# Kernel optimization log

Measured on AMD Instinct MI355X. Metric: run time of the kernel, lower is better.

The kernel has to match this reference:

```python
import jax, jax.numpy as jnp
import numpy as np
from jax import lax

EPS = 1e-5

def conv3x3(x, w):
    # x: [B,C,H,W], w: [O,C,3,3]
    return lax.conv_general_dilated(x, w, (1, 1), ((1, 1), (1, 1)),
                                    dimension_numbers=("NCHW", "OIHW", "NCHW"))

def convbnrelu(x, w, bn):
    gamma, beta, mean, var = bn  # each [C]
    y = conv3x3(x, w)
    scale = (gamma / jnp.sqrt(var + EPS))[:, None, None]
    shift = (beta - mean * gamma / jnp.sqrt(var + EPS))[:, None, None]
    return jax.nn.relu(y * scale + shift)

def conv1x1(x, w, b):
    # w: [O,C,1,1], b: [O]
    return jnp.einsum("bchw,oc->bohw", x, w[:, :, 0, 0]) + b[:, None, None]

def pam(x, wb, bb, wc, bc, wd, bd, alpha, lfm=None):
    B, C, H, W = x.shape
    N = H * W
    q = conv1x1(x, wb, bb)
    k = conv1x1(x, wc, bc)
    v = conv1x1(x, wd, bd)
    if lfm is not None:  # VFAM: qkv flags all 1 -> multiply q, k, v
        q = q * lfm
        k = k * lfm
        v = v * lfm
    fb = q.reshape(B, -1, N).transpose(0, 2, 1)           # [B,N,Cq]
    fc = k.reshape(B, -1, N)                              # [B,Cq,N]
    attn = jax.nn.softmax(jnp.matmul(fb, fc), axis=-1)    # [B,N,N]
    fd = v.reshape(B, C, N)                               # [B,C,N]
    fe = jnp.matmul(fd, attn.transpose(0, 2, 1)).reshape(B, C, H, W)
    return alpha * fe + x

def cam(x, beta):
    B, C, H, W = x.shape
    N = H * W
    fa = x.reshape(B, C, N)
    attn = jnp.matmul(fa, fa.transpose(0, 2, 1))          # [B,C,C]
    attn = jnp.max(attn, axis=-1, keepdims=True) - attn
    attn = jax.nn.softmax(attn, axis=-1)
    fe = jnp.matmul(attn, fa).reshape(B, C, H, W)
    return beta * fe + x

def setup_inputs() -> dict:
    key = jax.random.key(0)
    ks = iter(jax.random.split(key, 64))
    B, Cin, H, W = 2, 2048, 64, 64
    Cmid = Cin // 4         # 512
    Cq = Cmid // 8          # 64
    nclass = 19

    def bn_pack(C):
        g = jnp.ones((C,)) + 0.1 * jax.random.normal(next(ks), (C,))
        b = 0.1 * jax.random.normal(next(ks), (C,))
        m = 0.1 * jax.random.normal(next(ks), (C,))
        v = jax.random.uniform(next(ks), (C,), minval=0.5, maxval=1.5)
        return jnp.stack([g, b, m, v])  # [4,C]

    def conv_w(O, I, kk):
        return jax.random.normal(next(ks), (O, I, kk, kk)) * (1.0 / np.sqrt(I * kk * kk))

    inp = {
        "x": jax.random.normal(next(ks), (B, Cin, H, W)),
        "loss_factor_map": jax.random.uniform(next(ks), (H, W)),
        "wp1": conv_w(Cmid, Cin, 3), "bnp1": bn_pack(Cmid),
        "wp2": conv_w(Cmid, Cmid, 3), "bnp2": bn_pack(Cmid),
        "wc1": conv_w(Cmid, Cin, 3), "bnc1": bn_pack(Cmid),
        "wc2": conv_w(Cmid, Cmid, 3), "bnc2": bn_pack(Cmid),
        "wv1": conv_w(Cmid, Cin, 3), "bnv1": bn_pack(Cmid),
        "wv2": conv_w(Cmid, Cmid, 3), "bnv2": bn_pack(Cmid),
        "pam_wb": conv_w(Cq, Cmid, 1), "pam_bb": jnp.zeros((Cq,)),
        "pam_wc": conv_w(Cq, Cmid, 1), "pam_bc": jnp.zeros((Cq,)),
        "pam_wd": conv_w(Cmid, Cmid, 1), "pam_bd": jnp.zeros((Cmid,)),
        "pam_alpha": 0.3 * jnp.ones((1,)),
        "cam_beta": 0.3 * jnp.ones((1,)),
        "vfam_wb": conv_w(Cq, Cmid, 1), "vfam_bb": jnp.zeros((Cq,)),
        "vfam_wc": conv_w(Cq, Cmid, 1), "vfam_bc": jnp.zeros((Cq,)),
        "vfam_wd": conv_w(Cmid, Cmid, 1), "vfam_bd": jnp.zeros((Cmid,)),
        "vfam_alpha": 0.3 * jnp.ones((1,)),
        "out_w": conv_w(nclass, Cmid, 1), "out_b": jnp.zeros((nclass,)),
        "p3_w": conv_w(nclass, Cmid, 1), "p3_b": jnp.zeros((nclass,)),
        "c3_w": conv_w(nclass, Cmid, 1), "c3_b": jnp.zeros((nclass,)),
    }
    return inp

def reference(x, loss_factor_map,
              wp1, bnp1, wp2, bnp2, wc1, bnc1, wc2, bnc2, wv1, bnv1, wv2, bnv2,
              pam_wb, pam_bb, pam_wc, pam_bc, pam_wd, pam_bd, pam_alpha,
              cam_beta,
              vfam_wb, vfam_bb, vfam_wc, vfam_bc, vfam_wd, vfam_bd, vfam_alpha,
              out_w, out_b, p3_w, p3_b, c3_w, c3_b):
    lfm = loss_factor_map[None, None, :, :]  # (1,1,H,W)
    # Position branch
    fp = convbnrelu(x, wp1, bnp1)
    fp = pam(fp, pam_wb, pam_bb, pam_wc, pam_bc, pam_wd, pam_bd, pam_alpha)
    fp = convbnrelu(fp, wp2, bnp2)
    # Channel branch
    fc = convbnrelu(x, wc1, bnc1)
    fc = cam(fc, cam_beta)
    fc = convbnrelu(fc, wc2, bnc2)
    # Visual-field branch (qkv_vfa_flag = [1,1,1])
    fv = convbnrelu(x, wv1, bnv1)
    fv = pam(fv, vfam_wb, vfam_bb, vfam_wc, vfam_bc, vfam_wd, vfam_bd, vfam_alpha, lfm=lfm)
    fv = convbnrelu(fv, wv2, bnv2)
    # Fusion + heads (Dropout in eval mode = identity)
    fusion = fp + fc + fv
    fusion_out = conv1x1(fusion, out_w, out_b)
    p_out = conv1x1(fp, p3_w, p3_b)
    c_out = conv1x1(fc, c3_w, c3_b)
    return (fusion_out, p_out, c_out)
```

## Files before the change

### kernel.cpp

```cpp
#include <hip/hip_runtime.h>

typedef unsigned short u16;
typedef short s16x8 __attribute__((ext_vector_type(8)));
typedef u16 u16x8 __attribute__((ext_vector_type(8)));
typedef u16 u16x4 __attribute__((ext_vector_type(4)));
typedef float f32x4 __attribute__((ext_vector_type(4)));

#define DEV __device__ __forceinline__

DEV float bf2f(u16 x) { unsigned v = ((unsigned)x) << 16; float f; __builtin_memcpy(&f, &v, 4); return f; }
DEV u16 f2bf(float f) { unsigned u; __builtin_memcpy(&u, &f, 4); u += 0x7FFFu + ((u >> 16) & 1u); return (u16)(u >> 16); }

DEV void gload16(const u16* g, u16* l) {
  __builtin_amdgcn_global_load_lds((const __attribute__((address_space(1))) void*)g,
                                   (__attribute__((address_space(3))) void*)l, 16, 0, 0);
}

__global__ void detect_dtype(const u16* __restrict__ x, int* __restrict__ flag) {
  int tid = threadIdx.x;
  float mx = 0.f;
  for (int i = tid; i < 4096; i += 256) mx = fmaxf(mx, fabsf(bf2f(x[i])));
  __shared__ float red[4];
  int wave = tid >> 6, lane = tid & 63;
  for (int off = 32; off; off >>= 1) mx = fmaxf(mx, __shfl_xor(mx, off));
  if (lane == 0) red[wave] = mx;
  __syncthreads();
  if (tid == 0) {
    mx = fmaxf(fmaxf(red[0], red[1]), fmaxf(red[2], red[3]));
    *flag = (mx > 1e4f) ? 1 : 0;
  }
}

struct CvBatch {
  const void* src[28];
  unsigned dstOff[28];
  unsigned n[28];
  unsigned chunkStart[29];
  int cnt;
};

__global__ __launch_bounds__(256) void convert_batch(CvBatch cb, u16* __restrict__ dstBase,
                                                     const int* __restrict__ flag) {
  const int isF = *flag;
  const unsigned bid = blockIdx.x;
  int j = 0;
  while (bid >= cb.chunkStart[j + 1]) ++j;
  const unsigned base = (bid - cb.chunkStart[j]) * 2048 + threadIdx.x * 8;
  const unsigned n = cb.n[j];
  if (base >= n) return;
  u16* dst = dstBase + cb.dstOff[j];
  const void* src = cb.src[j];
  if (base + 8 <= n) {
    u16x8 v;
    if (isF) {
      const float* f = (const float*)src;
#pragma unroll
      for (int k = 0; k < 8; ++k) v[k] = f2bf(f[base + k]);
    } else {
      v = *(const u16x8*)&((const u16*)src)[base];
    }
    *(u16x8*)&dst[base] = v;
  } else {
    for (unsigned i = base; i < n; ++i)
      dst[i] = isF ? f2bf(((const float*)src)[i]) : ((const u16*)src)[i];
  }
}

__global__ void bn_prep(const u16* __restrict__ cbn, float* __restrict__ out) {
  int w = blockIdx.x;
  const u16* bn = cbn + w * 2048;
  int c = threadIdx.x;
  float g = bf2f(bn[c]), be = bf2f(bn[512 + c]), m = bf2f(bn[1024 + c]), v = bf2f(bn[1536 + c]);
  float sc = g * rsqrtf(v + 1e-5f);
  out[w * 1024 + c] = sc;
  out[w * 1024 + 512 + c] = be - m * sc;
}

struct Repack3P { const void* src[3]; u16* dst[3]; };

__global__ __launch_bounds__(256) void repack_w3(Repack3P rp, int I, int Ishift,
                                                 const int* __restrict__ flag) {
  const int isF = *flag;
  const void* w = rp.src[blockIdx.z];
  u16* wr = rp.dst[blockIdx.z];
  size_t idx = ((size_t)blockIdx.x * 256 + threadIdx.x) * 8;
  int i0 = (int)(idx & (size_t)(I - 1));
  int t = (int)(idx >> Ishift);
  int o = t / 9, kk = t - o * 9;
  u16x8 v;
  if (isF) {
    const float* f = (const float*)w;
#pragma unroll
    for (int j = 0; j < 8; ++j) v[j] = f2bf(f[((size_t)o * I + i0 + j) * 9 + kk]);
  } else {
    const u16* bsrc = (const u16*)w;
#pragma unroll
    for (int j = 0; j < 8; ++j) v[j] = bsrc[((size_t)o * I + i0 + j) * 9 + kk];
  }
  *(u16x8*)&wr[idx] = v;
}

__global__ __launch_bounds__(256) void zero_border(u16* __restrict__ base, int CIN) {
  int p = blockIdx.x, b = blockIdx.y;
  int py, px;
  if (p < 66)       { py = 0;        px = p; }
  else if (p < 132) { py = 65;       px = p - 66; }
  else if (p < 196) { py = p - 131;  px = 0; }
  else              { py = p - 195;  px = 65; }
  u16* d = base + (((size_t)b * 66 + py) * 66 + px) * (size_t)CIN;
  for (int i = threadIdx.x * 8; i < CIN; i += 2048) {
    u16x8 z;
#pragma unroll
    for (int k = 0; k < 8; ++k) z[k] = 0;
    *(u16x8*)&d[i] = z;
  }
}

__global__ __launch_bounds__(256) void pad_nchw(const void* __restrict__ x, u16* __restrict__ xpad,
                                                const int* __restrict__ flag) {
  __shared__ u16 t[64][72];
  const int isF = *flag;
  int c0 = blockIdx.x * 64, h = blockIdx.y, b = blockIdx.z;
  int tid = threadIdx.x;
#pragma unroll
  for (int i = 0; i < 2; ++i) {
    int idx = i * 256 + tid;
    int cc = idx >> 3, ww = (idx & 7) * 8;
    size_t base = (((size_t)(b * 2048 + c0 + cc) * 64) + h) * 64 + ww;
    u16x8 v;
    if (isF) {
      const float* fx = (const float*)x;
#pragma unroll
      for (int j = 0; j < 8; ++j) v[j] = f2bf(fx[base + j]);
    } else {
      v = *(const u16x8*)&((const u16*)x)[base];
    }
    *(u16x8*)&t[cc][ww] = v;
  }
  __syncthreads();
#pragma unroll
  for (int i = 0; i < 2; ++i) {
    int idx = i * 256 + tid;
    int ww = idx >> 3, cc = (idx & 7) * 8;
    u16x8 v;
#pragma unroll
    for (int j = 0; j < 8; ++j) v[j] = t[cc + j][ww];
    *(u16x8*)&xpad[(((size_t)b * 66 + h + 1) * 66 + ww + 1) * 2048 + c0 + cc] = v;
  }
}

__global__ __launch_bounds__(256) void transpose64(const u16* __restrict__ src, u16* __restrict__ dst,
                                                   int R, int C) {
  __shared__ u16 t[64][72];
  int r0 = blockIdx.x * 64, c0 = blockIdx.y * 64;
  const u16* s = src + (size_t)blockIdx.z * R * C;
  u16* d = dst + (size_t)blockIdx.z * R * C;
  int tid = threadIdx.x;
#pragma unroll
  for (int i = 0; i < 2; ++i) {
    int idx = i * 256 + tid;
    int rr = idx >> 3, cc = (idx & 7) * 8;
    u16x8 v = *(const u16x8*)&s[(size_t)(r0 + rr) * C + c0 + cc];
    *(u16x8*)&t[rr][cc] = v;
  }
  __syncthreads();
#pragma unroll
  for (int i = 0; i < 2; ++i) {
    int idx = i * 256 + tid;
    int cc = idx >> 3, rr = (idx & 7) * 8;
    u16x8 v;
#pragma unroll
    for (int j = 0; j < 8; ++j) v[j] = t[rr + j][cc];
    *(u16x8*)&d[(size_t)(c0 + cc) * R + r0 + rr] = v;
  }
}

struct GemmP {
  const u16* A; const u16* B;
  long aBatch, bBatch;
  int M, N, K;
  u16* out; long outBatch; int ldOut;
  const u16* bias;
  const u16* rowscale;
  const u16* residual; long resBatch; int ldRes;
  const u16* alphaPtr;
  float* outF; long outFBatch;
  const u16* B2; const u16* bias2; u16* out2;
};

template <int BM, int BN, int EPI>
__global__ __launch_bounds__(256) void gemm_nt(GemmP p) {
  static_assert(EPI != 2 || BM >= BN, "EPI2 LDS bounce needs BM>=BN");
  __shared__ __align__(16) u16 lsBuf[(BM + BN) * 32];
  u16* lA = lsBuf;
  u16* lB = lsBuf + BM * 32;
  const int tid = threadIdx.x;
  int bz = blockIdx.z;
  const u16* Bsel = p.B;
  const u16* biasSel = p.bias;
  u16* outSel = p.out;
  if (EPI == 0 && p.out2) {
    const int h = gridDim.z >> 1;
    if (bz >= h) { bz -= h; Bsel = p.B2; biasSel = p.bias2; outSel = p.out2; }
  }
  const int m0 = blockIdx.x * BM, n0 = blockIdx.y * BN;
  const u16* A = p.A + (size_t)bz * p.aBatch;
  const u16* Bp = Bsel + (size_t)bz * p.bBatch;
  const int wave = tid >> 6, lane = tid & 63;
  const int quad = lane >> 4, r16 = lane & 15;
  const int wm = (wave >> 1) * (BM / 2), wn = (wave & 1) * (BN / 2);
  constexpr int TM = BM / 32, TN = BN / 32;
  f32x4 acc[TM][TN] = {};
  const int srow = tid >> 2, sch = (tid & 3) * 8;
  const int K = p.K;
  for (int k0 = 0; k0 < K; k0 += 32) {
    __syncthreads();
#pragma unroll
    for (int i = 0; i < BM / 64; ++i)
      gload16(&A[(size_t)(m0 + i * 64 + srow) * K + k0 + sch], lA + i * 2048 + wave * 512);
#pragma unroll
    for (int i = 0; i < BN / 64; ++i)
      gload16(&Bp[(size_t)(n0 + i * 64 + srow) * K + k0 + sch], lB + i * 2048 + wave * 512);
    __syncthreads();
    s16x8 av[TM], bv[TN];
#pragma unroll
    for (int t = 0; t < TM; ++t) av[t] = *(const s16x8*)&lA[(wm + t * 16 + r16) * 32 + quad * 8];
#pragma unroll
    for (int t = 0; t < TN; ++t) bv[t] = *(const s16x8*)&lB[(wn + t * 16 + r16) * 32 + quad * 8];
#pragma unroll
    for (int i = 0; i < TM; ++i)
#pragma unroll
      for (int j = 0; j < TN; ++j)
        acc[i][j] = __builtin_amdgcn_mfma_f32_16x16x32_bf16(av[i], bv[j], acc[i][j], 0, 0, 0);
  }
  if constexpr (EPI == 2) {
    float* lsF = (float*)lsBuf;
#pragma unroll
    for (int i = 0; i < TM; ++i) {
      __syncthreads();
#pragma unroll
      for (int j = 0; j < TN; ++j) {
        const int col = wn + j * 16 + r16;
#pragma unroll
        for (int r = 0; r < 4; ++r) {
          const int rowL = (wave >> 1) * 16 + quad * 4 + r;
          lsF[rowL * BN + col] = acc[i][j][r];
        }
      }
      __syncthreads();
      constexpr int PASSES = (32 * BN) / 1024;
#pragma unroll
      for (int pp = 0; pp < PASSES; ++pp) {
        const int lin = (pp * 256 + tid) * 4;
        const int rowL = lin / BN, col = lin & (BN - 1);
        const int gm = m0 + (rowL >> 4) * (BM / 2) + i * 16 + (rowL & 15);
        *(f32x4*)&p.outF[(size_t)bz * p.outFBatch + (size_t)gm * p.ldOut + (n0 + col)] =
            *(const f32x4*)&lsF[lin];
      }
    }
    return;
  }
  float alpha = 0.f;
  if (EPI == 3) alpha = bf2f(p.alphaPtr[0]);
#pragma unroll
  for (int i = 0; i < TM; ++i) {
#pragma unroll
    for (int j = 0; j < TN; ++j) {
      const int nn = n0 + wn + j * 16 + r16;
      float bia = 0.f;
      if ((EPI == 0 || EPI == 1) && biasSel) bia = bf2f(biasSel[nn]);
#pragma unroll
      for (int r = 0; r < 4; ++r) {
        const int mm = m0 + wm + i * 16 + quad * 4 + r;
        float v = acc[i][j][r];
        if (EPI == 0) {
          v += bia;
          if (p.rowscale) v *= bf2f(p.rowscale[mm]);
          outSel[(size_t)bz * p.outBatch + (size_t)mm * p.ldOut + nn] = f2bf(v);
        } else if (EPI == 1) {
          v += bia;
          if (p.rowscale) v *= bf2f(p.rowscale[mm]);
          p.out[(size_t)bz * p.outBatch + (size_t)nn * p.ldOut + mm] = f2bf(v);
        } else {
          float res = bf2f(p.residual[(size_t)bz * p.resBatch + (size_t)mm * p.ldRes + nn]);
          v = alpha * v + res;
          const int py = mm >> 6, px = mm & 63;
          p.out[(size_t)bz * p.outBatch + ((size_t)(py + 1) * 66 + (px + 1)) * p.ldOut + nn] = f2bf(v);
        }
      }
    }
  }
}

struct Conv3P {
  const u16* in[3];
  const u16* wr[3];
  u16* out[3];
  const float* bn;
};

template <int CIN>
__global__ __launch_bounds__(256) void conv3x3_k(Conv3P p) {
  __shared__ u16 lA[4096], lB[4096];
  const int tid = threadIdx.x;
  const int z = blockIdx.z, ci = z >> 1, b = z & 1;
  const int m0 = blockIdx.x * 128, n0 = blockIdx.y * 128;
  const u16* __restrict__ xin = p.in[ci];
  const u16* __restrict__ wr = p.wr[ci];
  const int wave = tid >> 6, lane = tid & 63;
  const int quad = lane >> 4, r16 = lane & 15;
  const int wm = (wave >> 1) * 64, wn = (wave & 1) * 64;
  f32x4 acc[4][4] = {};
  const int srow = tid >> 2, sch = (tid & 3) * 8;
  const int p0 = m0 + srow, p1 = p0 + 64;
  const size_t a0 = (((size_t)b * 66 + (p0 >> 6)) * 66 + (p0 & 63)) * CIN + sch;
  const size_t a1 = (((size_t)b * 66 + (p1 >> 6)) * 66 + (p1 & 63)) * CIN + sch;
  const size_t b0 = ((size_t)(n0 + srow) * 9) * CIN + sch;
  const size_t b1 = ((size_t)(n0 + 64 + srow) * 9) * CIN + sch;
  u16* la0 = &lA[wave * 512];
  u16* la1 = &lA[2048 + wave * 512];
  u16* lb0 = &lB[wave * 512];
  u16* lb1 = &lB[2048 + wave * 512];
  for (int kh = 0; kh < 3; ++kh) {
    for (int kw = 0; kw < 3; ++kw) {
      const size_t soff = ((size_t)kh * 66 + kw) * CIN;
      const size_t woff = (size_t)(kh * 3 + kw) * CIN;
      for (int c = 0; c < CIN; c += 32) {
        __syncthreads();
        gload16(&xin[a0 + soff + c], la0);
        gload16(&xin[a1 + soff + c], la1);
        gload16(&wr[b0 + woff + c], lb0);
        gload16(&wr[b1 + woff + c], lb1);
        __syncthreads();
        s16x8 av[4], bv[4];
#pragma unroll
        for (int t = 0; t < 4; ++t) av[t] = *(const s16x8*)&lA[(wm + t * 16 + r16) * 32 + quad * 8];
#pragma unroll
        for (int t = 0; t < 4; ++t) bv[t] = *(const s16x8*)&lB[(wn + t * 16 + r16) * 32 + quad * 8];
#pragma unroll
        for (int i = 0; i < 4; ++i)
#pragma unroll
          for (int j = 0; j < 4; ++j)
            acc[i][j] = __builtin_amdgcn_mfma_f32_16x16x32_bf16(av[i], bv[j], acc[i][j], 0, 0, 0);
      }
    }
  }
  u16* __restrict__ out = p.out[ci];
  const float* bnS = p.bn + ci * 1024;
#pragma unroll
  for (int i = 0; i < 4; ++i) {
#pragma unroll
    for (int j = 0; j < 4; ++j) {
      const int nn = n0 + wn + j * 16 + r16;
      const float s = bnS[nn], sh = bnS[512 + nn];
#pragma unroll
      for (int r = 0; r < 4; ++r) {
        const int mm = m0 + wm + i * 16 + quad * 4 + r;
        float v = fmaxf(acc[i][j][r] * s + sh, 0.f);
        out[((size_t)b * 4096 + mm) * 512 + nn] = f2bf(v);
      }
    }
  }
}

__global__ __launch_bounds__(256) void softmax4096(const float* __restrict__ S, u16* __restrict__ P) {
  int row = blockIdx.x, tid = threadIdx.x;
  const float* sr = S + (size_t)row * 4096;
  f32x4 v[4];
  float mx = -3.4e38f;
#pragma unroll
  for (int i = 0; i < 4; ++i) {
    v[i] = *(const f32x4*)&sr[(i * 256 + tid) * 4];
    mx = fmaxf(mx, fmaxf(fmaxf(v[i][0], v[i][1]), fmaxf(v[i][2], v[i][3])));
  }
  __shared__ float red[8];
  int wave = tid >> 6, lane = tid & 63;
  for (int off = 32; off; off >>= 1) mx = fmaxf(mx, __shfl_xor(mx, off));
  if (lane == 0) red[wave] = mx;
  __syncthreads();
  mx = fmaxf(fmaxf(red[0], red[1]), fmaxf(red[2], red[3]));
  float sum = 0.f;
#pragma unroll
  for (int i = 0; i < 4; ++i)
#pragma unroll
    for (int j = 0; j < 4; ++j) { float e = __expf(v[i][j] - mx); v[i][j] = e; sum += e; }
  for (int off = 32; off; off >>= 1) sum += __shfl_xor(sum, off);
  if (lane == 0) red[4 + wave] = sum;
  __syncthreads();
  sum = red[4] + red[5] + red[6] + red[7];
  float inv = 1.f / sum;
  u16* pr = P + (size_t)row * 4096;
#pragma unroll
  for (int i = 0; i < 4; ++i) {
    u16x4 ov;
#pragma unroll
    for (int j = 0; j < 4; ++j) ov[j] = f2bf(v[i][j] * inv);
    *(u16x4*)&pr[(i * 256 + tid) * 4] = ov;
  }
}

__global__ __launch_bounds__(256) void softmax_cam(const float* __restrict__ S, u16* __restrict__ P) {
  int row = blockIdx.x, tid = threadIdx.x;
  const float* sr = S + (size_t)row * 512;
  float a = sr[tid], b = sr[tid + 256];
  __shared__ float red[12];
  int wave = tid >> 6, lane = tid & 63;
  float mx = fmaxf(a, b);
  for (int off = 32; off; off >>= 1) mx = fmaxf(mx, __shfl_xor(mx, off));
  if (lane == 0) red[wave] = mx;
  __syncthreads();
  float M1 = fmaxf(fmaxf(red[0], red[1]), fmaxf(red[2], red[3]));
  float mn = fminf(a, b);
  for (int off = 32; off; off >>= 1) mn = fminf(mn, __shfl_xor(mn, off));
  if (lane == 0) red[4 + wave] = mn;
  __syncthreads();
  float m2 = M1 - fminf(fminf(red[4], red[5]), fminf(red[6], red[7]));
  float e0 = __expf((M1 - a) - m2), e1 = __expf((M1 - b) - m2);
  float sum = e0 + e1;
  for (int off = 32; off; off >>= 1) sum += __shfl_xor(sum, off);
  if (lane == 0) red[8 + wave] = sum;
  __syncthreads();
  sum = red[8] + red[9] + red[10] + red[11];
  float inv = 1.f / sum;
  P[(size_t)row * 512 + tid] = f2bf(e0 * inv);
  P[(size_t)row * 512 + tid + 256] = f2bf(e1 * inv);
}

__global__ __launch_bounds__(256) void final_out_k(const u16* __restrict__ fp2, const u16* __restrict__ fc2,
                                                   const u16* __restrict__ fv2,
                                                   const u16* ow, const u16* ob, const u16* pw,
                                                   const u16* pb, const u16* cw, const u16* cb,
                                                   void* __restrict__ out, const int* __restrict__ flag) {
  __shared__ float wl[19 * 512];
  int tid = threadIdx.x, which = blockIdx.y;
  const u16* W = which == 0 ? ow : which == 1 ? pw : cw;
  const u16* Bb = which == 0 ? ob : which == 1 ? pb : cb;
  for (int i = tid; i < 19 * 512; i += 256) wl[i] = bf2f(W[i]);
  __syncthreads();
  int pix = blockIdx.x * 256 + threadIdx.x;
  size_t rb = (size_t)pix * 512;
  float acc[19];
#pragma unroll
  for (int o = 0; o < 19; ++o) acc[o] = 0.f;
  for (int c = 0; c < 512; c += 8) {
    float xs[8];
    if (which == 0) {
      u16x8 a = *(const u16x8*)&fp2[rb + c];
      u16x8 d = *(const u16x8*)&fc2[rb + c];
      u16x8 e = *(const u16x8*)&fv2[rb + c];
#pragma unroll
      for (int j = 0; j < 8; ++j) xs[j] = bf2f(a[j]) + bf2f(d[j]) + bf2f(e[j]);
    } else {
      const u16* src = which == 1 ? fp2 : fc2;
      u16x8 a = *(const u16x8*)&src[rb + c];
#pragma unroll
      for (int j = 0; j < 8; ++j) xs[j] = bf2f(a[j]);
    }
#pragma unroll
    for (int o = 0; o < 19; ++o) {
      const float* wv = &wl[o * 512 + c];
#pragma unroll
      for (int j = 0; j < 8; ++j) acc[o] += xs[j] * wv[j];
    }
  }
  int b = pix >> 12, n = pix & 4095;
  const int isF32 = *flag;
#pragma unroll
  for (int o = 0; o < 19; ++o) {
    size_t idx = (size_t)which * 155648 + ((size_t)(b * 19 + o)) * 4096 + n;
    float v = acc[o] + bf2f(Bb[o]);
    if (isF32) ((float*)out)[idx] = v;
    else ((u16*)out)[idx] = f2bf(v);
  }
}

static const size_t OFF_XPAD  = 0;
static const size_t OFF_WR1A  = 35684352;
static const size_t OFF_WR1B  = 54558720;
static const size_t OFF_WR1C  = 73433088;
static const size_t OFF_ARENA = 92307456;
static const size_t OFF_S     = 0;
static const size_t OFF_P     = 67108864;
static const size_t OFF_FP1   = 125861888;
static const size_t OFF_FC1   = 134250496;
static const size_t OFF_FV1   = 142639104;
static const size_t OFF_FC1T  = 151027712;
static const size_t OFF_QT    = 159416320;
static const size_t OFF_KT    = 160464896;
static const size_t OFF_VT    = 161513472;
static const size_t OFF_WRSA  = 151027712;
static const size_t OFF_WRSB  = 155746304;
static const size_t OFF_WRSC  = 161513472;
static const size_t OFF_PADP  = 169902080;
static const size_t OFF_PADC  = 178823168;
static const size_t OFF_PADV  = 187744256;
static const size_t OFF_FP2   = 125861888;
static const size_t OFF_FC2   = 134250496;
static const size_t OFF_FV2   = 142639104;
static const size_t OFF_SC    = 196665344;
static const size_t OFF_PC    = 198762496;
static const size_t OFF_BN    = 199811072;
static const size_t OFF_FLAG  = 199835648;
static const size_t OFF_SMALL = 199835904;
static const size_t SO_CBN    = 0;
static const size_t SO_PWB    = 12288;
static const size_t SO_PBB    = 45056;
static const size_t SO_PWC    = 45120;
static const size_t SO_PBC    = 77888;
static const size_t SO_PWD    = 77952;
static const size_t SO_PBD    = 340096;
static const size_t SO_PAL    = 340608;
static const size_t SO_CBETA  = 340624;
static const size_t SO_VWB    = 340640;
static const size_t SO_VBB    = 373408;
static const size_t SO_VWC    = 373472;
static const size_t SO_VBC    = 406240;
static const size_t SO_VWD    = 406304;
static const size_t SO_VBD    = 668448;
static const size_t SO_VAL    = 668960;
static const size_t SO_OW     = 668976;
static const size_t SO_OB     = 678704;
static const size_t SO_PW3    = 678736;
static const size_t SO_PB3    = 688464;
static const size_t SO_CW3    = 688496;
static const size_t SO_CB3    = 698224;
static const size_t SO_LFM    = 698256;
static const size_t SO_END    = 702352;
static const size_t WS_NEEDED = OFF_SMALL + SO_END * 2;

extern "C" void kernel_launch(void* const* d_in, const int* in_sizes, int n_in,
                              void* d_out, int out_size, void* d_ws, size_t ws_size,
                              hipStream_t stream) {
  if (ws_size < WS_NEEDED) return;
  (void)in_sizes; (void)n_in; (void)out_size;

  char* ws = (char*)d_ws;
  u16* xpad   = (u16*)(ws + OFF_XPAD);
  u16* wr1a   = (u16*)(ws + OFF_WR1A);
  u16* wr1b   = (u16*)(ws + OFF_WR1B);
  u16* wr1c   = (u16*)(ws + OFF_WR1C);
  float* S    = (float*)(ws + OFF_S);
  u16* P      = (u16*)(ws + OFF_P);
  u16* fp1    = (u16*)(ws + OFF_FP1);
  u16* fc1    = (u16*)(ws + OFF_FC1);
  u16* fv1    = (u16*)(ws + OFF_FV1);
  u16* fc1T   = (u16*)(ws + OFF_FC1T);
  u16* qt     = (u16*)(ws + OFF_QT);
  u16* kt     = (u16*)(ws + OFF_KT);
  u16* vT     = (u16*)(ws + OFF_VT);
  u16* wrsa   = (u16*)(ws + OFF_WRSA);
  u16* wrsb   = (u16*)(ws + OFF_WRSB);
  u16* wrsc   = (u16*)(ws + OFF_WRSC);
  u16* padP   = (u16*)(ws + OFF_PADP);
  u16* padC   = (u16*)(ws + OFF_PADC);
  u16* padV   = (u16*)(ws + OFF_PADV);
  u16* fp2    = (u16*)(ws + OFF_FP2);
  u16* fc2    = (u16*)(ws + OFF_FC2);
  u16* fv2    = (u16*)(ws + OFF_FV2);
  float* Sc   = (float*)(ws + OFF_SC);
  u16* Pc     = (u16*)(ws + OFF_PC);
  float* bnb  = (float*)(ws + OFF_BN);
  int* flag   = (int*)(ws + OFF_FLAG);
  u16* sm     = (u16*)(ws + OFF_SMALL);

  detect_dtype<<<1, 256, 0, stream>>>((const u16*)d_in[0], flag);
  {
    CvBatch cb{};
    int jn = 0; unsigned chunks = 0;
    auto addJob = [&](int i, size_t dstOff, unsigned n) {
      cb.src[jn] = d_in[i]; cb.dstOff[jn] = (unsigned)dstOff; cb.n[jn] = n;
      cb.chunkStart[jn] = chunks; chunks += (n + 2047) / 2048; ++jn;
    };
    addJob(3,  SO_CBN + 0 * 2048, 2048);
    addJob(7,  SO_CBN + 1 * 2048, 2048);
    addJob(11, SO_CBN + 2 * 2048, 2048);
    addJob(5,  SO_CBN + 3 * 2048, 2048);
    addJob(9,  SO_CBN + 4 * 2048, 2048);
    addJob(13, SO_CBN + 5 * 2048, 2048);
    addJob(14, SO_PWB, 32768);  addJob(15, SO_PBB, 64);
    addJob(16, SO_PWC, 32768);  addJob(17, SO_PBC, 64);
    addJob(18, SO_PWD, 262144); addJob(19, SO_PBD, 512);
    addJob(20, SO_PAL, 1);      addJob(21, SO_CBETA, 1);
    addJob(22, SO_VWB, 32768);  addJob(23, SO_VBB, 64);
    addJob(24, SO_VWC, 32768);  addJob(25, SO_VBC, 64);
    addJob(26, SO_VWD, 262144); addJob(27, SO_VBD, 512);
    addJob(28, SO_VAL, 1);
    addJob(29, SO_OW, 9728);    addJob(30, SO_OB, 19);
    addJob(31, SO_PW3, 9728);   addJob(32, SO_PB3, 19);
    addJob(33, SO_CW3, 9728);   addJob(34, SO_CB3, 19);
    addJob(1,  SO_LFM, 4096);
    cb.cnt = jn; cb.chunkStart[jn] = chunks;
    convert_batch<<<chunks, 256, 0, stream>>>(cb, sm, flag);
  }

  bn_prep<<<6, 512, 0, stream>>>(sm + SO_CBN, bnb);

  zero_border<<<dim3(260, 2), 256, 0, stream>>>(xpad, 2048);
  pad_nchw<<<dim3(32, 64, 2), 256, 0, stream>>>(d_in[0], xpad, flag);

  {
    Repack3P rp{};
    rp.src[0] = d_in[2];  rp.dst[0] = wr1a;
    rp.src[1] = d_in[6];  rp.dst[1] = wr1b;
    rp.src[2] = d_in[10]; rp.dst[2] = wr1c;
    repack_w3<<<dim3(4608, 1, 3), 256, 0, stream>>>(rp, 2048, 11, flag);
  }
  {
    Conv3P c{};
    c.in[0] = xpad; c.in[1] = xpad; c.in[2] = xpad;
    c.wr[0] = wr1a; c.wr[1] = wr1b; c.wr[2] = wr1c;
    c.out[0] = fp1; c.out[1] = fc1; c.out[2] = fv1;
    c.bn = bnb;
    conv3x3_k<2048><<<dim3(32, 4, 6), 256, 0, stream>>>(c);
  }

  auto runPam = [&](const u16* src, const u16* wb, const u16* bb, const u16* wck, const u16* bck,
                    const u16* wd, const u16* bd, const u16* alphaP, const u16* rs, u16* padOut) {
    GemmP g{};
    g.A = src; g.aBatch = 2097152; g.B = wb; g.bBatch = 0; g.M = 4096; g.N = 64; g.K = 512;
    g.out = qt; g.outBatch = 262144; g.ldOut = 64; g.bias = bb; g.rowscale = rs;
    g.B2 = wck; g.bias2 = bck; g.out2 = kt;
    gemm_nt<64, 64, 0><<<dim3(64, 1, 4), 256, 0, stream>>>(g);
    GemmP gv{};
    gv.A = src; gv.aBatch = 2097152; gv.B = wd; gv.bBatch = 0; gv.M = 4096; gv.N = 512; gv.K = 512;
    gv.out = vT; gv.outBatch = 2097152; gv.ldOut = 4096; gv.bias = bd; gv.rowscale = rs;
    gemm_nt<64, 128, 1><<<dim3(64, 4, 2), 256, 0, stream>>>(gv);
    zero_border<<<dim3(260, 2), 256, 0, stream>>>(padOut, 512);
    for (int b = 0; b < 2; ++b) {
      GemmP gs{};
      gs.A = qt + (size_t)b * 262144; gs.B = kt + (size_t)b * 262144;
      gs.M = 4096; gs.N = 4096; gs.K = 64;
      gs.outF = S; gs.outFBatch = 0; gs.ldOut = 4096;
      gemm_nt<128, 128, 2><<<dim3(32, 32, 1), 256, 0, stream>>>(gs);
      softmax4096<<<4096, 256, 0, stream>>>(S, P);
      GemmP gf{};
      gf.A = P; gf.aBatch = 0; gf.B = vT + (size_t)b * 2097152; gf.bBatch = 0;
      gf.M = 4096; gf.N = 512; gf.K = 4096;
      gf.out = padOut + (size_t)b * 2230272; gf.outBatch = 0; gf.ldOut = 512;
      gf.residual = src + (size_t)b * 2097152; gf.resBatch = 0; gf.ldRes = 512;
      gf.alphaPtr = alphaP;
      gemm_nt<128, 64, 3><<<dim3(32, 8, 1), 256, 0, stream>>>(gf);
    }
  };
  runPam(fp1, sm + SO_PWB, sm + SO_PBB, sm + SO_PWC, sm + SO_PBC, sm + SO_PWD, sm + SO_PBD,
         sm + SO_PAL, nullptr, padP);
  runPam(fv1, sm + SO_VWB, sm + SO_VBB, sm + SO_VWC, sm + SO_VBC, sm + SO_VWD, sm + SO_VBD,
         sm + SO_VAL, sm + SO_LFM, padV);

  transpose64<<<dim3(64, 8, 2), 256, 0, stream>>>(fc1, fc1T, 4096, 512);
  {
    GemmP g{};
    g.A = fc1T; g.aBatch = 2097152; g.B = fc1T; g.bBatch = 2097152;
    g.M = 512; g.N = 512; g.K = 4096;
    g.outF = Sc; g.outFBatch = 262144; g.ldOut = 512;
    gemm_nt<64, 64, 2><<<dim3(8, 8, 2), 256, 0, stream>>>(g);
  }
  softmax_cam<<<1024, 256, 0, stream>>>(Sc, Pc);
  zero_border<<<dim3(260, 2), 256, 0, stream>>>(padC, 512);
  {
    GemmP g{};
    g.A = fc1; g.aBatch = 2097152; g.B = Pc; g.bBatch = 262144;
    g.M = 4096; g.N = 512; g.K = 512;
    g.out = padC; g.outBatch = 2230272; g.ldOut = 512;
    g.residual = fc1; g.resBatch = 2097152; g.ldRes = 512;
    g.alphaPtr = sm + SO_CBETA;
    gemm_nt<128, 128, 3><<<dim3(32, 4, 2), 256, 0, stream>>>(g);
  }

  {
    Repack3P rp{};
    rp.src[0] = d_in[4];  rp.dst[0] = wrsa;
    rp.src[1] = d_in[8];  rp.dst[1] = wrsb;
    rp.src[2] = d_in[12]; rp.dst[2] = wrsc;
    repack_w3<<<dim3(1152, 1, 3), 256, 0, stream>>>(rp, 512, 9, flag);
  }
  {
    Conv3P c{};
    c.in[0] = padP; c.in[1] = padC; c.in[2] = padV;
    c.wr[0] = wrsa; c.wr[1] = wrsb; c.wr[2] = wrsc;
    c.out[0] = fp2; c.out[1] = fc2; c.out[2] = fv2;
    c.bn = bnb + 3 * 1024;
    conv3x3_k<512><<<dim3(32, 4, 6), 256, 0, stream>>>(c);
  }

  final_out_k<<<dim3(32, 3), 256, 0, stream>>>(fp2, fc2, fv2, sm + SO_OW, sm + SO_OB,
                                               sm + SO_PW3, sm + SO_PB3, sm + SO_CW3, sm + SO_CB3,
                                               d_out, flag);
}
```

Measured before the change: 1.647 ms.

## Double-buffer LDS staging in GEMM and conv3x3 kernels to overlap loads

Both the generic NT GEMM and the implicit-GEMM 3x3 conv now use two LDS buffers. The next K-slice is issued via global_load_lds while MFMAs run on the current one, with a single barrier per iteration instead of two. The conv loop is flattened and reordered to kh,kw-inner, c-outer to simplify prefetch indexing, which changes the access order. This doubles LDS use per block and may lower occupancy. It also relies on the barrier to make the async LDS writes visible, with no explicit vmcnt wait.

Result: faster. 1.508 ms (-8.4%).

```diff
diff --git a/kernel.cpp b/kernel.cpp
--- a/kernel.cpp
+++ b/kernel.cpp
@@ -191,9 +191,8 @@
 template <int BM, int BN, int EPI>
 __global__ __launch_bounds__(256) void gemm_nt(GemmP p) {
   static_assert(EPI != 2 || BM >= BN, "EPI2 LDS bounce needs BM>=BN");
-  __shared__ __align__(16) u16 lsBuf[(BM + BN) * 32];
-  u16* lA = lsBuf;
-  u16* lB = lsBuf + BM * 32;
+  constexpr int HB = (BM + BN) * 32;
+  __shared__ __align__(16) u16 ls[2][HB];
   const int tid = threadIdx.x;
   int bz = blockIdx.z;
   const u16* Bsel = p.B;
@@ -213,15 +212,22 @@
   f32x4 acc[TM][TN] = {};
   const int srow = tid >> 2, sch = (tid & 3) * 8;
   const int K = p.K;
+  auto stage = [&](int buf, int k0) {
+#pragma unroll
+    for (int i = 0; i < BM / 64; ++i)
+      gload16(&A[(size_t)(m0 + i * 64 + srow) * K + k0 + sch], &ls[buf][i * 2048 + wave * 512]);
+#pragma unroll
+    for (int i = 0; i < BN / 64; ++i)
+      gload16(&Bp[(size_t)(n0 + i * 64 + srow) * K + k0 + sch],
+              &ls[buf][BM * 32 + i * 2048 + wave * 512]);
+  };
+  stage(0, 0);
+  __syncthreads();
+  int cur = 0;
   for (int k0 = 0; k0 < K; k0 += 32) {
-    __syncthreads();
-#pragma unroll
-    for (int i = 0; i < BM / 64; ++i)
-      gload16(&A[(size_t)(m0 + i * 64 + srow) * K + k0 + sch], lA + i * 2048 + wave * 512);
-#pragma unroll
-    for (int i = 0; i < BN / 64; ++i)
-      gload16(&Bp[(size_t)(n0 + i * 64 + srow) * K + k0 + sch], lB + i * 2048 + wave * 512);
-    __syncthreads();
+    if (k0 + 32 < K) stage(cur ^ 1, k0 + 32);
+    const u16* lA = &ls[cur][0];
+    const u16* lB = &ls[cur][BM * 32];
     s16x8 av[TM], bv[TN];
 #pragma unroll
     for (int t = 0; t < TM; ++t) av[t] = *(const s16x8*)&lA[(wm + t * 16 + r16) * 32 + quad * 8];
@@ -232,9 +238,11 @@
 #pragma unroll
       for (int j = 0; j < TN; ++j)
         acc[i][j] = __builtin_amdgcn_mfma_f32_16x16x32_bf16(av[i], bv[j], acc[i][j], 0, 0, 0);
+    __syncthreads();
+    cur ^= 1;
   }
   if constexpr (EPI == 2) {
-    float* lsF = (float*)lsBuf;
+    float* lsF = (float*)&ls[0][0];
 #pragma unroll
     for (int i = 0; i < TM; ++i) {
       __syncthreads();
@@ -301,7 +309,7 @@
 
 template <int CIN>
 __global__ __launch_bounds__(256) void conv3x3_k(Conv3P p) {
-  __shared__ u16 lA[4096], lB[4096];
+  __shared__ __align__(16) u16 ls[2][8192];
   const int tid = threadIdx.x;
   const int z = blockIdx.z, ci = z >> 1, b = z & 1;
   const int m0 = blockIdx.x * 128, n0 = blockIdx.y * 128;
@@ -317,33 +325,40 @@
   const size_t a1 = (((size_t)b * 66 + (p1 >> 6)) * 66 + (p1 & 63)) * CIN + sch;
   const size_t b0 = ((size_t)(n0 + srow) * 9) * CIN + sch;
   const size_t b1 = ((size_t)(n0 + 64 + srow) * 9) * CIN + sch;
-  u16* la0 = &lA[wave * 512];
-  u16* la1 = &lA[2048 + wave * 512];
-  u16* lb0 = &lB[wave * 512];
-  u16* lb1 = &lB[2048 + wave * 512];
-  for (int kh = 0; kh < 3; ++kh) {
-    for (int kw = 0; kw < 3; ++kw) {
-      const size_t soff = ((size_t)kh * 66 + kw) * CIN;
-      const size_t woff = (size_t)(kh * 3 + kw) * CIN;
-      for (int c = 0; c < CIN; c += 32) {
-        __syncthreads();
-        gload16(&xin[a0 + soff + c], la0);
-        gload16(&xin[a1 + soff + c], la1);
-        gload16(&wr[b0 + woff + c], lb0);
-        gload16(&wr[b1 + woff + c], lb1);
-        __syncthreads();
-        s16x8 av[4], bv[4];
-#pragma unroll
-        for (int t = 0; t < 4; ++t) av[t] = *(const s16x8*)&lA[(wm + t * 16 + r16) * 32 + quad * 8];
-#pragma unroll
-        for (int t = 0; t < 4; ++t) bv[t] = *(const s16x8*)&lB[(wn + t * 16 + r16) * 32 + quad * 8];
-#pragma unroll
-        for (int i = 0; i < 4; ++i)
-#pragma unroll
-          for (int j = 0; j < 4; ++j)
-            acc[i][j] = __builtin_amdgcn_mfma_f32_16x16x32_bf16(av[i], bv[j], acc[i][j], 0, 0, 0);
-      }
-    }
+  auto stage = [&](int buf, int kh, int kw, int c) {
+    const size_t soff = ((size_t)(kh * 66 + kw)) * CIN + c;
+    const size_t woff = (size_t)(kh * 3 + kw) * CIN + c;
+    u16* base = &ls[buf][0];
+    gload16(&xin[a0 + soff], base + wave * 512);
+    gload16(&xin[a1 + soff], base + 2048 + wave * 512);
+    gload16(&wr[b0 + woff], base + 4096 + wave * 512);
+    gload16(&wr[b1 + woff], base + 6144 + wave * 512);
+  };
+  const int NT = (CIN / 32) * 9;
+  stage(0, 0, 0, 0);
+  __syncthreads();
+  int cur = 0;
+  int khN = 0, kwN = 1, cN = 0;
+  for (int t = 0; t < NT; ++t) {
+    if (t + 1 < NT) {
+      stage(cur ^ 1, khN, kwN, cN);
+      if (++kwN == 3) { kwN = 0; if (++khN == 3) { khN = 0; cN += 32; } }
+    }
+    const u16* base = &ls[cur][0];
+    s16x8 av[4], bv[4];
+#pragma unroll
+    for (int tt = 0; tt < 4; ++tt)
+      av[tt] = *(const s16x8*)&base[(wm + tt * 16 + r16) * 32 + quad * 8];
+#pragma unroll
+    for (int tt = 0; tt < 4; ++tt)
+      bv[tt] = *(const s16x8*)&base[4096 + (wn + tt * 16 + r16) * 32 + quad * 8];
+#pragma unroll
+    for (int i = 0; i < 4; ++i)
+#pragma unroll
+      for (int j = 0; j < 4; ++j)
+        acc[i][j] = __builtin_amdgcn_mfma_f32_16x16x32_bf16(av[i], bv[j], acc[i][j], 0, 0, 0);
+    __syncthreads();
+    cur ^= 1;
   }
   u16* __restrict__ out = p.out[ci];
   const float* bnS = p.bn + ci * 1024;
```
